# Optimization experiments

Measured on AMD Instinct MI355X. Metric: run time of the kernel, lower is better.

Reference implementation:

```python
import jax, jax.numpy as jnp
import numpy as np

N, E, S, G = 20000, 60000, 3000, 128
EAD = 5
DIMS = [(16, 32), (32, 64), (64, 64)]  # NNConv (M_in, M_out) per layer
HID = 128  # edge-MLP hidden
FC_IN = 64 + 8  # conv output + raw continuous feats


def setup_inputs() -> dict:
    key = jax.random.key(0)
    ks = iter(jax.random.split(key, 64))
    inp = {}
    inp['x'] = jax.random.normal(next(ks), (N, 24), jnp.float32)
    inp['edge_index'] = jax.random.randint(next(ks), (2, E), 0, N)
    inp['edge_attr'] = jax.random.uniform(next(ks), (E, EAD), jnp.float32)
    inp['node_to_subgraph'] = jnp.sort(jax.random.randint(next(ks), (N,), 0, S))
    inp['subgraph_to_graph'] = jnp.sort(jax.random.randint(next(ks), (S,), 0, G))
    for i, (mi, mo) in enumerate(DIMS):
        inp[f'conv{i}_w1'] = jax.random.normal(next(ks), (EAD, HID), jnp.float32) / np.sqrt(EAD)
        inp[f'conv{i}_b1'] = jnp.zeros((HID,), jnp.float32)
        inp[f'conv{i}_w2'] = jax.random.normal(next(ks), (HID, mi * mo), jnp.float32) / np.sqrt(HID * mi)
        inp[f'conv{i}_b2'] = jnp.zeros((mi * mo,), jnp.float32)
        inp[f'conv{i}_root'] = jax.random.normal(next(ks), (mi, mo), jnp.float32) / np.sqrt(mi)
        inp[f'conv{i}_bias'] = jnp.zeros((mo,), jnp.float32)
    dims_fc = [(FC_IN, FC_IN // 2), (FC_IN // 2, FC_IN // 4), (FC_IN // 4, 1)]
    for i, (di, do) in enumerate(dims_fc):
        inp[f'fc{i+1}_w'] = jax.random.normal(next(ks), (di, do), jnp.float32) / np.sqrt(di)
        inp[f'fc{i+1}_b'] = jnp.zeros((do,), jnp.float32)
    return inp


def _nnconv(x, src, dst, ea, w1, b1, w2, b2, root, bias):
    # edge MLP -> per-edge weight matrix [E, M_in, M_out]
    h = jax.nn.relu(ea @ w1 + b1)
    mi, mo = root.shape
    W = (h @ w2 + b2).reshape(-1, mi, mo)
    msg = jnp.einsum('ei,eio->eo', x[src], W)  # gather + per-edge matmul
    agg = jax.ops.segment_sum(msg, dst, num_segments=x.shape[0])  # scatter-add
    return agg + x @ root + bias


def _mean_pool(x, seg, num):
    s = jax.ops.segment_sum(x, seg, num_segments=num)
    c = jax.ops.segment_sum(jnp.ones((x.shape[0], 1), x.dtype), seg, num_segments=num)
    return s / jnp.maximum(c, 1.0)


def _forward(x, edge_index, edge_attr, node_to_subgraph, subgraph_to_graph, convs, fcs):
    src, dst = edge_index[0], edge_index[1]
    xi = x[:, :16]
    for p in convs:
        xi = jax.nn.elu(_nnconv(xi, src, dst, edge_attr, *p))
    x_cont = x[:, 16:]
    xc = jnp.concatenate([xi, x_cont], axis=1)  # [N, 72]
    xs = _mean_pool(xc, node_to_subgraph, S)    # [S, 72]
    xg = _mean_pool(xs, subgraph_to_graph, G)   # [G, 72]
    (w1, b1), (w2, b2), (w3, b3) = fcs
    xg = jax.nn.elu(xg @ w1 + b1)
    xg = jax.nn.elu(xg @ w2 + b2)
    return (xg @ w3 + b3).reshape(-1)


def reference(x, edge_index, edge_attr, node_to_subgraph, subgraph_to_graph,
              conv0_w1, conv0_b1, conv0_w2, conv0_b2, conv0_root, conv0_bias,
              conv1_w1, conv1_b1, conv1_w2, conv1_b2, conv1_root, conv1_bias,
              conv2_w1, conv2_b1, conv2_w2, conv2_b2, conv2_root, conv2_bias,
              fc1_w, fc1_b, fc2_w, fc2_b, fc3_w, fc3_b):
    convs = [
        (conv0_w1, conv0_b1, conv0_w2, conv0_b2, conv0_root, conv0_bias),
        (conv1_w1, conv1_b1, conv1_w2, conv1_b2, conv1_root, conv1_bias),
        (conv2_w1, conv2_b1, conv2_w2, conv2_b2, conv2_root, conv2_bias),
    ]
    fcs = [(fc1_w, fc1_b), (fc2_w, fc2_b), (fc3_w, fc3_b)]
    return _forward(x, edge_index, edge_attr, node_to_subgraph, subgraph_to_graph, convs, fcs)
```

## Files before the change

### kernel.cpp

```cpp
#include <hip/hip_runtime.h>
#include <hip/hip_bf16.h>
#include <cmath>

#define NN 20000
#define NE 60000
#define NS 3000
#define NG 128
#define HIDN 128
#define SCB 79

typedef float f32x16 __attribute__((ext_vector_type(16)));
typedef _Float16 f16x8 __attribute__((ext_vector_type(8)));

__device__ __forceinline__ float eluf(float v) { return v > 0.f ? v : expm1f(v); }

__device__ __forceinline__ void gload_lds16(const void* g, void* l) {
    __builtin_amdgcn_global_load_lds(
        (const __attribute__((address_space(1))) unsigned int*)g,
        (__attribute__((address_space(3))) unsigned int*)l, 16, 0, 0);
}

template <int N> struct VmWait;
template <> struct VmWait<0>  { static __device__ __forceinline__ void run() { asm volatile("s_waitcnt vmcnt(0)"  ::: "memory"); } };
template <> struct VmWait<12> { static __device__ __forceinline__ void run() { asm volatile("s_waitcnt vmcnt(12)" ::: "memory"); } };
template <> struct VmWait<16> { static __device__ __forceinline__ void run() { asm volatile("s_waitcnt vmcnt(16)" ::: "memory"); } };
template <> struct VmWait<40> { static __device__ __forceinline__ void run() { asm volatile("s_waitcnt vmcnt(40)" ::: "memory"); } };

__global__ void k_hist(const int* __restrict__ dst, int* __restrict__ deg) {
    int e = blockIdx.x * 256 + threadIdx.x;
    if (e < NE) atomicAdd(&deg[dst[e]], 1);
}

__global__ void k_scan1(const int* __restrict__ deg, int* __restrict__ bsum) {
    __shared__ int s[256];
    const int t = threadIdx.x;
    int i = blockIdx.x * 256 + t;
    s[t] = (i < NN) ? deg[i] : 0;
    __syncthreads();
#pragma unroll
    for (int off = 128; off > 0; off >>= 1) {
        if (t < off) s[t] += s[t + off];
        __syncthreads();
    }
    if (t == 0) bsum[blockIdx.x] = s[0];
}

__global__ void k_scan2(const int* __restrict__ bsum, int* __restrict__ boff) {
    __shared__ int s[SCB];
    const int t = threadIdx.x;
    if (t < SCB) s[t] = bsum[t];
    __syncthreads();
    if (t == 0) {
        int acc = 0;
        for (int i = 0; i < SCB; ++i) { int v = s[i]; s[i] = acc; acc += v; }
    }
    __syncthreads();
    if (t < SCB) boff[t] = s[t];
}

__global__ void k_scan3(const int* __restrict__ deg, const int* __restrict__ boff,
                        int* __restrict__ rowptr) {
    __shared__ int s[256];
    const int t = threadIdx.x;
    int i = blockIdx.x * 256 + t;
    int v = (i < NN) ? deg[i] : 0;
    s[t] = v;
    __syncthreads();
#pragma unroll
    for (int off = 1; off < 256; off <<= 1) {
        int a = (t >= off) ? s[t - off] : 0;
        __syncthreads();
        s[t] += a;
        __syncthreads();
    }
    if (i < NN) rowptr[i + 1] = boff[blockIdx.x] + s[t];
    if (i == 0) rowptr[0] = 0;
}

__global__ void k_scatter(const int* __restrict__ src, const int* __restrict__ dst,
                          const int* __restrict__ rowptr, int* __restrict__ tmp,
                          int* __restrict__ eord, int* __restrict__ srcS) {
    int e = blockIdx.x * 256 + threadIdx.x;
    if (e >= NE) return;
    int d = dst[e];
    int pos = rowptr[d] + atomicAdd(&tmp[d], 1);
    eord[pos] = e;
    srcS[pos] = src[e];
}

__global__ void k_hT2(const int* __restrict__ eord, const float* __restrict__ ea,
                      const float* __restrict__ w1, const float* __restrict__ b1,
                      _Float16* __restrict__ hT) {
    __shared__ float sea[64][5];
    const int t  = threadIdx.x;
    const int eb = blockIdx.x * 64;
    for (int i = t; i < 320; i += 256) {
        int el = i / 5, d = i % 5;
        int es = eb + el;
        int e = (es < NE) ? eord[es] : 0;
        sea[el][d] = ea[e * 5 + d];
    }
    __syncthreads();
    const int w = t >> 6, lane = t & 63;
    const int es = eb + lane;
    const float a0 = sea[lane][0], a1 = sea[lane][1], a2 = sea[lane][2],
                a3 = sea[lane][3], a4 = sea[lane][4];
#pragma unroll 4
    for (int jj = 0; jj < 32; ++jj) {
        const int j = w * 32 + jj;
        float s = b1[j];
        s = fmaf(a0, w1[0 * HIDN + j], s);
        s = fmaf(a1, w1[1 * HIDN + j], s);
        s = fmaf(a2, w1[2 * HIDN + j], s);
        s = fmaf(a3, w1[3 * HIDN + j], s);
        s = fmaf(a4, w1[4 * HIDN + j], s);
        if (es < NE) hT[(size_t)j * NE + es] = (_Float16)fmaxf(s, 0.f);
    }
}

template <int MI, int MO>
__global__ void k_w2t(const float* __restrict__ w2, const float* __restrict__ b2,
                      _Float16* __restrict__ w2t) {
    constexpr int KP = 129 * MI;
    constexpr int KF = 128 * MI;
    int idx = blockIdx.x * 256 + threadIdx.x;
    if (idx >= MO * KP) return;
    int o = idx / KP, kg = idx % KP;
    float v = (kg < KF) ? w2[(size_t)kg * MO + o] : b2[(kg - KF) * MO + o];
    w2t[idx] = (_Float16)v;
}

__global__ void k_x16h(const float* __restrict__ x, _Float16* __restrict__ xh) {
    int idx = blockIdx.x * 256 + threadIdx.x;
    if (idx >= NN * 16) return;
    int n = idx >> 4, i = idx & 15;
    xh[idx] = (_Float16)x[n * 24 + i];
}

template <int MI, int MO, int XS>
__global__ __launch_bounds__(256, 2) void k_edge6(
    const _Float16* __restrict__ xi, const _Float16* __restrict__ hT,
    const _Float16* __restrict__ w2t, const int* __restrict__ srcS,
    float* __restrict__ msg) {
    constexpr int PH  = MI / 16;
    constexpr int KP  = 129 * MI;
    constexpr int NT  = MO / 32;
    constexpr int CH  = 16 / (PH * NT);
    constexpr int NCH = 64 / CH;
    constexpr int VMK = 8 + 2 * CH;
    static_assert(CH * PH * NT == 16, "ITEMS must be 16");

    __shared__ __align__(16) _Float16 sb[2][2][16 * 512];

    const int lane = threadIdx.x & 63;
    const int w    = threadIdx.x >> 6;
    const int mg   = w & 1;
    const int kh   = w >> 1;
    const int lo5  = lane & 31;
    const int hi   = lane >> 5;
    const int e0   = blockIdx.x * 128 + mg * 64;
    const int kb   = kh * 64;

    const int rc0 = min(e0 + lo5, NE - 1);
    const int rc1 = min(e0 + 32 + lo5, NE - 1);
    const int s0 = srcS[rc0];
    const int s1 = srcS[rc1];

    f16x8 xr0[PH], xr1[PH];
    {
        const _Float16* xb0 = xi + (size_t)s0 * XS + hi * 8;
        const _Float16* xb1 = xi + (size_t)s1 * XS + hi * 8;
#pragma unroll
        for (int p = 0; p < PH; ++p) {
            xr0[p] = *reinterpret_cast<const f16x8*>(xb0 + p * 16);
            xr1[p] = *reinterpret_cast<const f16x8*>(xb1 + p * 16);
        }
    }

    f32x16 acc[2][NT];
#pragma unroll
    for (int m = 0; m < 2; ++m)
#pragma unroll
        for (int n = 0; n < NT; ++n)
#pragma unroll
            for (int i = 0; i < 16; ++i) acc[m][n][i] = 0.f;

    auto stage = [&](int buf, int kc) {
#pragma unroll
        for (int jj = 0; jj < 8; ++jj) {
            const int j  = mg + jj * 2;
            const int n  = j % NT;
            const int kp = j / NT;
            const int p  = kp % PH;
            const int kk = kp / PH;
            gload_lds16(w2t + (size_t)(n * 32 + lo5) * KP
                            + (size_t)(kb + kc + kk) * MI + p * 16 + hi * 8,
                        &sb[kh][buf][j * 512]);
        }
    };

    _Float16 hc0[CH], hc1[CH], hn0[CH], hn1[CH];

    stage(0, 0);
#pragma unroll
    for (int kk = 0; kk < CH; ++kk) {
        hc0[kk] = hT[(size_t)(kb + kk) * NE + rc0];
        hc1[kk] = hT[(size_t)(kb + kk) * NE + rc1];
    }

    for (int c = 0; c < NCH; ++c) {
        const bool pf = (c + 1 < NCH);
        if (pf) {
            stage((c + 1) & 1, (c + 1) * CH);
#pragma unroll
            for (int kk = 0; kk < CH; ++kk) {
                hn0[kk] = hT[(size_t)(kb + (c + 1) * CH + kk) * NE + rc0];
                hn1[kk] = hT[(size_t)(kb + (c + 1) * CH + kk) * NE + rc1];
            }
        }
        if (pf) VmWait<VMK>::run(); else VmWait<0>::run();
        __builtin_amdgcn_s_barrier();
        __builtin_amdgcn_sched_barrier(0);
        asm volatile("" ::: "memory");

        const _Float16* sbc = &sb[kh][c & 1][0];
#pragma unroll
        for (int kk = 0; kk < CH; ++kk) {
            const _Float16 hv0 = hc0[kk];
            const _Float16 hv1 = hc1[kk];
            const f16x8 h80 = {hv0, hv0, hv0, hv0, hv0, hv0, hv0, hv0};
            const f16x8 h81 = {hv1, hv1, hv1, hv1, hv1, hv1, hv1, hv1};
#pragma unroll
            for (int p = 0; p < PH; ++p) {
                const f16x8 af0 = xr0[p] * h80;
                const f16x8 af1 = xr1[p] * h81;
#pragma unroll
                for (int n = 0; n < NT; ++n) {
                    const f16x8 bv = *reinterpret_cast<const f16x8*>(
                        &sbc[((kk * PH + p) * NT + n) * 512 + lane * 8]);
                    acc[0][n] = __builtin_amdgcn_mfma_f32_32x32x16_f16(af0, bv, acc[0][n], 0, 0, 0);
                    acc[1][n] = __builtin_amdgcn_mfma_f32_32x32x16_f16(af1, bv, acc[1][n], 0, 0, 0);
                }
            }
        }
        __builtin_amdgcn_sched_barrier(0);
        asm volatile("" ::: "memory");
        __builtin_amdgcn_s_barrier();
        if (pf) {
#pragma unroll
            for (int kk = 0; kk < CH; ++kk) { hc0[kk] = hn0[kk]; hc1[kk] = hn1[kk]; }
        }
    }

    if (kh == 1) {
#pragma unroll
        for (int p = 0; p < PH; ++p) {
#pragma unroll
            for (int n = 0; n < NT; ++n) {
                const f16x8 bv = *reinterpret_cast<const f16x8*>(
                    w2t + (size_t)(n * 32 + lo5) * KP + (size_t)128 * MI + p * 16 + hi * 8);
                acc[0][n] = __builtin_amdgcn_mfma_f32_32x32x16_f16(xr0[p], bv, acc[0][n], 0, 0, 0);
                acc[1][n] = __builtin_amdgcn_mfma_f32_32x32x16_f16(xr1[p], bv, acc[1][n], 0, 0, 0);
            }
        }
    }

    __syncthreads();
    float* red = reinterpret_cast<float*>(&sb[0][0][0]);
    if (kh == 1) {
#pragma unroll
        for (int m = 0; m < 2; ++m)
#pragma unroll
            for (int n = 0; n < NT; ++n) {
                float* d = red + (size_t)((mg * 2 + m) * NT + n) * 1024 + lane;
#pragma unroll
                for (int i = 0; i < 16; ++i) d[i * 64] = acc[m][n][i];
            }
    }
    __syncthreads();
    if (kh == 0) {
#pragma unroll
        for (int m = 0; m < 2; ++m)
#pragma unroll
            for (int n = 0; n < NT; ++n) {
                const float* s = red + (size_t)((mg * 2 + m) * NT + n) * 1024 + lane;
#pragma unroll
                for (int i = 0; i < 16; ++i) acc[m][n][i] += s[i * 64];
            }
#pragma unroll
        for (int m = 0; m < 2; ++m)
#pragma unroll
            for (int q = 0; q < 4; ++q)
#pragma unroll
                for (int a = 0; a < 4; ++a) {
                    const int e = e0 + m * 32 + 4 * hi + 8 * q + a;
                    if (e < NE) {
#pragma unroll
                        for (int n = 0; n < NT; ++n)
                            msg[(size_t)e * MO + n * 32 + lo5] = acc[m][n][4 * q + a];
                    }
                }
    }
}

template <int MI, int MO, int XS>
__global__ void k_agg(const float* __restrict__ msg, const int* __restrict__ rowptr,
                      const float* __restrict__ xi, const float* __restrict__ root,
                      const float* __restrict__ bias, float* __restrict__ out,
                      _Float16* __restrict__ outh) {
    int idx = blockIdx.x * 256 + threadIdx.x;
    if (idx >= NN * MO) return;
    int n = idx / MO, o = idx % MO;
    float s = bias[o];
#pragma unroll
    for (int i = 0; i < MI; ++i) s = fmaf(xi[(size_t)n * XS + i], root[i * MO + o], s);
    const int j0 = rowptr[n], j1 = rowptr[n + 1];
    for (int j = j0; j < j1; ++j) s += msg[(size_t)j * MO + o];
    float r = eluf(s);
    out[idx] = r;
    outh[idx] = (_Float16)r;
}

__global__ void k_pool_s(const float* __restrict__ xi, const float* __restrict__ x,
                         const int* __restrict__ n2s, float* __restrict__ xs_sum,
                         float* __restrict__ cs) {
    int idx = blockIdx.x * 256 + threadIdx.x;
    if (idx >= NN * 72) return;
    int n = idx / 72, j = idx % 72;
    float v = (j < 64) ? xi[n * 64 + j] : x[n * 24 + 16 + (j - 64)];
    int s = n2s[n];
    atomicAdd(&xs_sum[s * 72 + j], v);
    if (j == 0) atomicAdd(&cs[s], 1.f);
}

__global__ void k_pool_g(const float* __restrict__ xs_sum, const float* __restrict__ cs,
                         const int* __restrict__ s2g, float* __restrict__ xg_sum,
                         float* __restrict__ cg) {
    int idx = blockIdx.x * 256 + threadIdx.x;
    if (idx >= NS * 72) return;
    int s = idx / 72, j = idx % 72;
    float v = xs_sum[s * 72 + j] / fmaxf(cs[s], 1.f);
    int g = s2g[s];
    atomicAdd(&xg_sum[g * 72 + j], v);
    if (j == 0) atomicAdd(&cg[g], 1.f);
}

__global__ void k_fc(const float* __restrict__ xg_sum, const float* __restrict__ cg,
                     const float* __restrict__ w1, const float* __restrict__ b1,
                     const float* __restrict__ w2, const float* __restrict__ b2,
                     const float* __restrict__ w3, const float* __restrict__ b3,
                     float* __restrict__ out) {
    int g = threadIdx.x;
    if (g >= NG) return;
    float inv = 1.f / fmaxf(cg[g], 1.f);
    float v[72];
#pragma unroll
    for (int j = 0; j < 72; ++j) v[j] = xg_sum[g * 72 + j] * inv;
    float h1[36];
#pragma unroll
    for (int o = 0; o < 36; ++o) {
        float s = b1[o];
#pragma unroll
        for (int i = 0; i < 72; ++i) s = fmaf(v[i], w1[i * 36 + o], s);
        h1[o] = eluf(s);
    }
    float h2[18];
#pragma unroll
    for (int o = 0; o < 18; ++o) {
        float s = b2[o];
#pragma unroll
        for (int i = 0; i < 36; ++i) s = fmaf(h1[i], w2[i * 18 + o], s);
        h2[o] = eluf(s);
    }
    float s = b3[0];
#pragma unroll
    for (int i = 0; i < 18; ++i) s = fmaf(h2[i], w3[i], s);
    out[g] = s;
}

extern "C" void kernel_launch(void* const* d_in, const int* in_sizes, int n_in,
                              void* d_out, int out_size, void* d_ws, size_t ws_size,
                              hipStream_t stream) {
    const float* x   = (const float*)d_in[0];
    const int*   ei  = (const int*)d_in[1];
    const float* ea  = (const float*)d_in[2];
    const int*   n2s = (const int*)d_in[3];
    const int*   s2g = (const int*)d_in[4];
    const int* src = ei;
    const int* dst = ei + NE;

    const float* cw1[3]   = {(const float*)d_in[5],  (const float*)d_in[11], (const float*)d_in[17]};
    const float* cb1[3]   = {(const float*)d_in[6],  (const float*)d_in[12], (const float*)d_in[18]};
    const float* cw2[3]   = {(const float*)d_in[7],  (const float*)d_in[13], (const float*)d_in[19]};
    const float* cb2[3]   = {(const float*)d_in[8],  (const float*)d_in[14], (const float*)d_in[20]};
    const float* croot[3] = {(const float*)d_in[9],  (const float*)d_in[15], (const float*)d_in[21]};
    const float* cbias[3] = {(const float*)d_in[10], (const float*)d_in[16], (const float*)d_in[22]};
    const float* fc1w = (const float*)d_in[23];
    const float* fc1b = (const float*)d_in[24];
    const float* fc2w = (const float*)d_in[25];
    const float* fc2b = (const float*)d_in[26];
    const float* fc3w = (const float*)d_in[27];
    const float* fc3b = (const float*)d_in[28];

    char* W = (char*)d_ws;
    _Float16* hT    = (_Float16*)(W);
    float*    xiA   = (float*)(W + 15360000);
    float*    xiB   = (float*)(W + 20480000);
    _Float16* xiAh  = (_Float16*)(W + 25600000);
    _Float16* xiBh  = (_Float16*)(W + 28160000);
    _Float16* x16h  = (_Float16*)(W + 30720000);
    float*    msg   = (float*)(W + 31360000);
    float*    xs_sum= (float*)(W + 46720000);
    float*    cs    = (float*)(W + 47584000);
    float*    xg_sum= (float*)(W + 47596000);
    float*    cg    = (float*)(W + 47632864);
    _Float16* w2t0  = (_Float16*)(W + 47633376);
    _Float16* w2t1  = (_Float16*)(W + 47765472);
    _Float16* w2t2  = (_Float16*)(W + 48293856);
    int*      deg   = (int*)(W + 49350624);
    int*      tmp   = (int*)(W + 49430624);
    int*      rowptr= (int*)(W + 49510624);
    int*      eord  = (int*)(W + 49590640);
    int*      srcS  = (int*)(W + 49830640);
    int*      bsum  = (int*)(W + 50070640);
    int*      boff  = (int*)(W + 50070960);

    hipMemsetAsync(xs_sum, 0, (size_t)(NS * 72 + NS) * 4 + (size_t)(NG * 72 + NG) * 4, stream);
    hipMemsetAsync(deg, 0, 160000, stream);

    k_hist<<<(NE + 255) / 256, 256, 0, stream>>>(dst, deg);
    k_scan1<<<SCB, 256, 0, stream>>>(deg, bsum);
    k_scan2<<<1, 128, 0, stream>>>(bsum, boff);
    k_scan3<<<SCB, 256, 0, stream>>>(deg, boff, rowptr);
    k_scatter<<<(NE + 255) / 256, 256, 0, stream>>>(src, dst, rowptr, tmp, eord, srcS);

    k_w2t<16, 32><<<(32 * 129 * 16 + 255) / 256, 256, 0, stream>>>(cw2[0], cb2[0], w2t0);
    k_w2t<32, 64><<<(64 * 129 * 32 + 255) / 256, 256, 0, stream>>>(cw2[1], cb2[1], w2t1);
    k_w2t<64, 64><<<(64 * 129 * 64 + 255) / 256, 256, 0, stream>>>(cw2[2], cb2[2], w2t2);
    k_x16h<<<(NN * 16 + 255) / 256, 256, 0, stream>>>(x, x16h);

    const int EB = (NE + 127) / 128;
    const int HTB = (NE + 63) / 64;

    k_hT2<<<HTB, 256, 0, stream>>>(eord, ea, cw1[0], cb1[0], hT);
    k_edge6<16, 32, 16><<<EB, 256, 0, stream>>>(x16h, hT, w2t0, srcS, msg);
    k_agg<16, 32, 24><<<(NN * 32 + 255) / 256, 256, 0, stream>>>(msg, rowptr, x, croot[0], cbias[0], xiB, xiBh);

    k_hT2<<<HTB, 256, 0, stream>>>(eord, ea, cw1[1], cb1[1], hT);
    k_edge6<32, 64, 32><<<EB, 256, 0, stream>>>(xiBh, hT, w2t1, srcS, msg);
    k_agg<32, 64, 32><<<(NN * 64 + 255) / 256, 256, 0, stream>>>(msg, rowptr, xiB, croot[1], cbias[1], xiA, xiAh);

    k_hT2<<<HTB, 256, 0, stream>>>(eord, ea, cw1[2], cb1[2], hT);
    k_edge6<64, 64, 64><<<EB, 256, 0, stream>>>(xiAh, hT, w2t2, srcS, msg);
    k_agg<64, 64, 64><<<(NN * 64 + 255) / 256, 256, 0, stream>>>(msg, rowptr, xiA, croot[2], cbias[2], xiB, xiBh);

    k_pool_s<<<(NN * 72 + 255) / 256, 256, 0, stream>>>(xiB, x, n2s, xs_sum, cs);
    k_pool_g<<<(NS * 72 + 255) / 256, 256, 0, stream>>>(xs_sum, cs, s2g, xg_sum, cg);
    k_fc<<<1, 128, 0, stream>>>(xg_sum, cg, fc1w, fc1b, fc2w, fc2b, fc3w, fc3b, (float*)d_out);
}
```

Before: 313.0 us.

## Split edge kernel output columns across grid y and double-buffer with unrolled loop

The per-edge MFMA kernel now computes only one 32-wide output tile per block, with the output-column tile index taken from blockIdx.y. This halves LDS staging and accumulator registers, which allows a launch bound of 4 blocks per SM instead of 2. The chunk loop is unrolled by two with fixed buffer indices, and the wait counts are adjusted to match. In exchange, the gather of x rows and of hT is repeated for each column tile, so layers with 64 outputs now read those inputs twice.

```diff
diff --git a/kernel.cpp b/kernel.cpp
--- a/kernel.cpp
+++ b/kernel.cpp
@@ -22,9 +22,9 @@
 
 template <int N> struct VmWait;
 template <> struct VmWait<0>  { static __device__ __forceinline__ void run() { asm volatile("s_waitcnt vmcnt(0)"  ::: "memory"); } };
+template <> struct VmWait<8>  { static __device__ __forceinline__ void run() { asm volatile("s_waitcnt vmcnt(8)"  ::: "memory"); } };
 template <> struct VmWait<12> { static __device__ __forceinline__ void run() { asm volatile("s_waitcnt vmcnt(12)" ::: "memory"); } };
-template <> struct VmWait<16> { static __device__ __forceinline__ void run() { asm volatile("s_waitcnt vmcnt(16)" ::: "memory"); } };
-template <> struct VmWait<40> { static __device__ __forceinline__ void run() { asm volatile("s_waitcnt vmcnt(40)" ::: "memory"); } };
+template <> struct VmWait<20> { static __device__ __forceinline__ void run() { asm volatile("s_waitcnt vmcnt(20)" ::: "memory"); } };
 
 __global__ void k_hist(const int* __restrict__ dst, int* __restrict__ deg) {
     int e = blockIdx.x * 256 + threadIdx.x;
@@ -138,19 +138,19 @@
 }
 
 template <int MI, int MO, int XS>
-__global__ __launch_bounds__(256, 2) void k_edge6(
+__global__ __launch_bounds__(256, 4) void k_edge7(
     const _Float16* __restrict__ xi, const _Float16* __restrict__ hT,
     const _Float16* __restrict__ w2t, const int* __restrict__ srcS,
     float* __restrict__ msg) {
     constexpr int PH  = MI / 16;
     constexpr int KP  = 129 * MI;
-    constexpr int NT  = MO / 32;
-    constexpr int CH  = 16 / (PH * NT);
+    constexpr int CH  = 8 / PH;
     constexpr int NCH = 64 / CH;
-    constexpr int VMK = 8 + 2 * CH;
-    static_assert(CH * PH * NT == 16, "ITEMS must be 16");
-
-    __shared__ __align__(16) _Float16 sb[2][2][16 * 512];
+    constexpr int VMK = 4 + 2 * CH;
+    static_assert(CH * PH == 8, "ITEMS must be 8");
+    static_assert(NCH % 2 == 0, "chunk loop unrolled x2");
+
+    __shared__ __align__(16) _Float16 sb[2][2][8 * 512];
 
     const int lane = threadIdx.x & 63;
     const int w    = threadIdx.x >> 6;
@@ -159,6 +159,7 @@
     const int lo5  = lane & 31;
     const int hi   = lane >> 5;
     const int e0   = blockIdx.x * 128 + mg * 64;
+    const int ns   = blockIdx.y;
     const int kb   = kh * 64;
 
     const int rc0 = min(e0 + lo5, NE - 1);
@@ -177,91 +178,92 @@
         }
     }
 
-    f32x16 acc[2][NT];
-#pragma unroll
-    for (int m = 0; m < 2; ++m)
-#pragma unroll
-        for (int n = 0; n < NT; ++n)
-#pragma unroll
-            for (int i = 0; i < 16; ++i) acc[m][n][i] = 0.f;
+    f32x16 acc0, acc1;
+#pragma unroll
+    for (int i = 0; i < 16; ++i) { acc0[i] = 0.f; acc1[i] = 0.f; }
+
+    const _Float16* bbase = w2t + (size_t)(ns * 32 + lo5) * KP + hi * 8;
 
     auto stage = [&](int buf, int kc) {
 #pragma unroll
-        for (int jj = 0; jj < 8; ++jj) {
+        for (int jj = 0; jj < 4; ++jj) {
             const int j  = mg + jj * 2;
-            const int n  = j % NT;
-            const int kp = j / NT;
-            const int p  = kp % PH;
-            const int kk = kp / PH;
-            gload_lds16(w2t + (size_t)(n * 32 + lo5) * KP
-                            + (size_t)(kb + kc + kk) * MI + p * 16 + hi * 8,
+            const int kk = j / PH;
+            const int p  = j % PH;
+            gload_lds16(bbase + (size_t)(kb + kc + kk) * MI + p * 16,
                         &sb[kh][buf][j * 512]);
         }
     };
 
-    _Float16 hc0[CH], hc1[CH], hn0[CH], hn1[CH];
-
-    stage(0, 0);
-#pragma unroll
-    for (int kk = 0; kk < CH; ++kk) {
-        hc0[kk] = hT[(size_t)(kb + kk) * NE + rc0];
-        hc1[kk] = hT[(size_t)(kb + kk) * NE + rc1];
-    }
-
-    for (int c = 0; c < NCH; ++c) {
-        const bool pf = (c + 1 < NCH);
-        if (pf) {
-            stage((c + 1) & 1, (c + 1) * CH);
-#pragma unroll
-            for (int kk = 0; kk < CH; ++kk) {
-                hn0[kk] = hT[(size_t)(kb + (c + 1) * CH + kk) * NE + rc0];
-                hn1[kk] = hT[(size_t)(kb + (c + 1) * CH + kk) * NE + rc1];
-            }
-        }
-        if (pf) VmWait<VMK>::run(); else VmWait<0>::run();
-        __builtin_amdgcn_s_barrier();
-        __builtin_amdgcn_sched_barrier(0);
-        asm volatile("" ::: "memory");
-
-        const _Float16* sbc = &sb[kh][c & 1][0];
+    auto compute = [&](int buf, const _Float16* h0, const _Float16* h1) {
+        const _Float16* sbc = &sb[kh][buf][0];
 #pragma unroll
         for (int kk = 0; kk < CH; ++kk) {
-            const _Float16 hv0 = hc0[kk];
-            const _Float16 hv1 = hc1[kk];
+            const _Float16 hv0 = h0[kk];
+            const _Float16 hv1 = h1[kk];
             const f16x8 h80 = {hv0, hv0, hv0, hv0, hv0, hv0, hv0, hv0};
             const f16x8 h81 = {hv1, hv1, hv1, hv1, hv1, hv1, hv1, hv1};
 #pragma unroll
             for (int p = 0; p < PH; ++p) {
                 const f16x8 af0 = xr0[p] * h80;
                 const f16x8 af1 = xr1[p] * h81;
-#pragma unroll
-                for (int n = 0; n < NT; ++n) {
-                    const f16x8 bv = *reinterpret_cast<const f16x8*>(
-                        &sbc[((kk * PH + p) * NT + n) * 512 + lane * 8]);
-                    acc[0][n] = __builtin_amdgcn_mfma_f32_32x32x16_f16(af0, bv, acc[0][n], 0, 0, 0);
-                    acc[1][n] = __builtin_amdgcn_mfma_f32_32x32x16_f16(af1, bv, acc[1][n], 0, 0, 0);
-                }
+                const f16x8 bv = *reinterpret_cast<const f16x8*>(
+                    &sbc[(kk * PH + p) * 512 + lane * 8]);
+                acc0 = __builtin_amdgcn_mfma_f32_32x32x16_f16(af0, bv, acc0, 0, 0, 0);
+                acc1 = __builtin_amdgcn_mfma_f32_32x32x16_f16(af1, bv, acc1, 0, 0, 0);
             }
         }
+    };
+
+    _Float16 hA0[CH], hA1[CH], hB0[CH], hB1[CH];
+
+    stage(0, 0);
+#pragma unroll
+    for (int kk = 0; kk < CH; ++kk) {
+        hA0[kk] = hT[(size_t)(kb + kk) * NE + rc0];
+        hA1[kk] = hT[(size_t)(kb + kk) * NE + rc1];
+    }
+
+    for (int c = 0; c < NCH; c += 2) {
+        stage(1, (c + 1) * CH);
+#pragma unroll
+        for (int kk = 0; kk < CH; ++kk) {
+            hB0[kk] = hT[(size_t)(kb + (c + 1) * CH + kk) * NE + rc0];
+            hB1[kk] = hT[(size_t)(kb + (c + 1) * CH + kk) * NE + rc1];
+        }
+        VmWait<VMK>::run();
+        __builtin_amdgcn_s_barrier();
         __builtin_amdgcn_sched_barrier(0);
-        asm volatile("" ::: "memory");
+        compute(0, hA0, hA1);
+        __builtin_amdgcn_sched_barrier(0);
         __builtin_amdgcn_s_barrier();
+
+        const bool pf = (c + 2 < NCH);
         if (pf) {
-#pragma unroll
-            for (int kk = 0; kk < CH; ++kk) { hc0[kk] = hn0[kk]; hc1[kk] = hn1[kk]; }
-        }
+            stage(0, (c + 2) * CH);
+#pragma unroll
+            for (int kk = 0; kk < CH; ++kk) {
+                hA0[kk] = hT[(size_t)(kb + (c + 2) * CH + kk) * NE + rc0];
+                hA1[kk] = hT[(size_t)(kb + (c + 2) * CH + kk) * NE + rc1];
+            }
+            VmWait<VMK>::run();
+        } else {
+            VmWait<0>::run();
+        }
+        __builtin_amdgcn_s_barrier();
+        __builtin_amdgcn_sched_barrier(0);
+        compute(1, hB0, hB1);
+        __builtin_amdgcn_sched_barrier(0);
+        __builtin_amdgcn_s_barrier();
     }
 
     if (kh == 1) {
 #pragma unroll
         for (int p = 0; p < PH; ++p) {
-#pragma unroll
-            for (int n = 0; n < NT; ++n) {
-                const f16x8 bv = *reinterpret_cast<const f16x8*>(
-                    w2t + (size_t)(n * 32 + lo5) * KP + (size_t)128 * MI + p * 16 + hi * 8);
-                acc[0][n] = __builtin_amdgcn_mfma_f32_32x32x16_f16(xr0[p], bv, acc[0][n], 0, 0, 0);
-                acc[1][n] = __builtin_amdgcn_mfma_f32_32x32x16_f16(xr1[p], bv, acc[1][n], 0, 0, 0);
-            }
+            const f16x8 bv = *reinterpret_cast<const f16x8*>(
+                bbase + (size_t)128 * MI + p * 16);
+            acc0 = __builtin_amdgcn_mfma_f32_32x32x16_f16(xr0[p], bv, acc0, 0, 0, 0);
+            acc1 = __builtin_amdgcn_mfma_f32_32x32x16_f16(xr1[p], bv, acc1, 0, 0, 0);
         }
     }
 
@@ -269,35 +271,32 @@
     float* red = reinterpret_cast<float*>(&sb[0][0][0]);
     if (kh == 1) {
 #pragma unroll
+        for (int m = 0; m < 2; ++m) {
+            float* d = red + (size_t)(mg * 2 + m) * 1024 + lane;
+            const f32x16& a = (m == 0) ? acc0 : acc1;
+#pragma unroll
+            for (int i = 0; i < 16; ++i) d[i * 64] = a[i];
+        }
+    }
+    __syncthreads();
+    if (kh == 0) {
+#pragma unroll
+        for (int m = 0; m < 2; ++m) {
+            const float* s = red + (size_t)(mg * 2 + m) * 1024 + lane;
+            f32x16& a = (m == 0) ? acc0 : acc1;
+#pragma unroll
+            for (int i = 0; i < 16; ++i) a[i] += s[i * 64];
+        }
+#pragma unroll
         for (int m = 0; m < 2; ++m)
 #pragma unroll
-            for (int n = 0; n < NT; ++n) {
-                float* d = red + (size_t)((mg * 2 + m) * NT + n) * 1024 + lane;
-#pragma unroll
-                for (int i = 0; i < 16; ++i) d[i * 64] = acc[m][n][i];
-            }
-    }
-    __syncthreads();
-    if (kh == 0) {
-#pragma unroll
-        for (int m = 0; m < 2; ++m)
-#pragma unroll
-            for (int n = 0; n < NT; ++n) {
-                const float* s = red + (size_t)((mg * 2 + m) * NT + n) * 1024 + lane;
-#pragma unroll
-                for (int i = 0; i < 16; ++i) acc[m][n][i] += s[i * 64];
-            }
-#pragma unroll
-        for (int m = 0; m < 2; ++m)
-#pragma unroll
             for (int q = 0; q < 4; ++q)
 #pragma unroll
-                for (int a = 0; a < 4; ++a) {
-                    const int e = e0 + m * 32 + 4 * hi + 8 * q + a;
+                for (int a2 = 0; a2 < 4; ++a2) {
+                    const int e = e0 + m * 32 + 4 * hi + 8 * q + a2;
                     if (e < NE) {
-#pragma unroll
-                        for (int n = 0; n < NT; ++n)
-                            msg[(size_t)e * MO + n * 32 + lo5] = acc[m][n][4 * q + a];
+                        const float v = (m == 0) ? acc0[4 * q + a2] : acc1[4 * q + a2];
+                        msg[(size_t)e * MO + ns * 32 + lo5] = v;
                     }
                 }
     }
@@ -443,15 +442,15 @@
     const int HTB = (NE + 63) / 64;
 
     k_hT2<<<HTB, 256, 0, stream>>>(eord, ea, cw1[0], cb1[0], hT);
-    k_edge6<16, 32, 16><<<EB, 256, 0, stream>>>(x16h, hT, w2t0, srcS, msg);
+    k_edge7<16, 32, 16><<<dim3(EB, 1), 256, 0, stream>>>(x16h, hT, w2t0, srcS, msg);
     k_agg<16, 32, 24><<<(NN * 32 + 255) / 256, 256, 0, stream>>>(msg, rowptr, x, croot[0], cbias[0], xiB, xiBh);
 
     k_hT2<<<HTB, 256, 0, stream>>>(eord, ea, cw1[1], cb1[1], hT);
-    k_edge6<32, 64, 32><<<EB, 256, 0, stream>>>(xiBh, hT, w2t1, srcS, msg);
+    k_edge7<32, 64, 32><<<dim3(EB, 2), 256, 0, stream>>>(xiBh, hT, w2t1, srcS, msg);
     k_agg<32, 64, 32><<<(NN * 64 + 255) / 256, 256, 0, stream>>>(msg, rowptr, xiB, croot[1], cbias[1], xiA, xiAh);
 
     k_hT2<<<HTB, 256, 0, stream>>>(eord, ea, cw1[2], cb1[2], hT);
-    k_edge6<64, 64, 64><<<EB, 256, 0, stream>>>(xiAh, hT, w2t2, srcS, msg);
+    k_edge7<64, 64, 64><<<dim3(EB, 2), 256, 0, stream>>>(xiAh, hT, w2t2, srcS, msg);
     k_agg<64, 64, 64><<<(NN * 64 + 255) / 256, 256, 0, stream>>>(msg, rowptr, xiA, croot[2], cbias[2], xiB, xiBh);
 
     k_pool_s<<<(NN * 72 + 255) / 256, 256, 0, stream>>>(xiB, x, n2s, xs_sum, cs);
```

Measured after the change: 329.9 us. 5.4% more time.

## Give each wave private LDS buffers and drop per-chunk block barriers in edge kernel

Applied to the files above, without the earlier changes.

Each wave now stages its own weight tiles into a private LDS region instead of sharing half-tiles with a partner wave, which removes the two workgroup barriers per chunk. The chunk size is halved to eight MFMA items and the loop is unrolled by two with explicit ping-pong buffers, relying only on per-wave vmcnt waits. This trades duplicated global-to-LDS traffic (each wave loads the full tile rather than half) for less synchronization and better latency hiding.

```diff
diff --git a/kernel.cpp b/kernel.cpp
--- a/kernel.cpp
+++ b/kernel.cpp
@@ -22,9 +22,9 @@
 
 template <int N> struct VmWait;
 template <> struct VmWait<0>  { static __device__ __forceinline__ void run() { asm volatile("s_waitcnt vmcnt(0)"  ::: "memory"); } };
+template <> struct VmWait<10> { static __device__ __forceinline__ void run() { asm volatile("s_waitcnt vmcnt(10)" ::: "memory"); } };
 template <> struct VmWait<12> { static __device__ __forceinline__ void run() { asm volatile("s_waitcnt vmcnt(12)" ::: "memory"); } };
-template <> struct VmWait<16> { static __device__ __forceinline__ void run() { asm volatile("s_waitcnt vmcnt(16)" ::: "memory"); } };
-template <> struct VmWait<40> { static __device__ __forceinline__ void run() { asm volatile("s_waitcnt vmcnt(40)" ::: "memory"); } };
+template <> struct VmWait<24> { static __device__ __forceinline__ void run() { asm volatile("s_waitcnt vmcnt(24)" ::: "memory"); } };
 
 __global__ void k_hist(const int* __restrict__ dst, int* __restrict__ deg) {
     int e = blockIdx.x * 256 + threadIdx.x;
@@ -138,19 +138,20 @@
 }
 
 template <int MI, int MO, int XS>
-__global__ __launch_bounds__(256, 2) void k_edge6(
+__global__ __launch_bounds__(256, 2) void k_edge8(
     const _Float16* __restrict__ xi, const _Float16* __restrict__ hT,
     const _Float16* __restrict__ w2t, const int* __restrict__ srcS,
     float* __restrict__ msg) {
     constexpr int PH  = MI / 16;
     constexpr int KP  = 129 * MI;
     constexpr int NT  = MO / 32;
-    constexpr int CH  = 16 / (PH * NT);
+    constexpr int CH  = 8 / (PH * NT);
     constexpr int NCH = 64 / CH;
     constexpr int VMK = 8 + 2 * CH;
-    static_assert(CH * PH * NT == 16, "ITEMS must be 16");
-
-    __shared__ __align__(16) _Float16 sb[2][2][16 * 512];
+    static_assert(CH * PH * NT == 8, "ITEMS must be 8");
+    static_assert(NCH % 2 == 0, "chunk loop unrolled x2");
+
+    __shared__ __align__(16) _Float16 sb[4][2][8 * 512];
 
     const int lane = threadIdx.x & 63;
     const int w    = threadIdx.x >> 6;
@@ -187,47 +188,23 @@
 
     auto stage = [&](int buf, int kc) {
 #pragma unroll
-        for (int jj = 0; jj < 8; ++jj) {
-            const int j  = mg + jj * 2;
+        for (int j = 0; j < 8; ++j) {
             const int n  = j % NT;
             const int kp = j / NT;
             const int p  = kp % PH;
             const int kk = kp / PH;
             gload_lds16(w2t + (size_t)(n * 32 + lo5) * KP
                             + (size_t)(kb + kc + kk) * MI + p * 16 + hi * 8,
-                        &sb[kh][buf][j * 512]);
+                        &sb[w][buf][j * 512]);
         }
     };
 
-    _Float16 hc0[CH], hc1[CH], hn0[CH], hn1[CH];
-
-    stage(0, 0);
-#pragma unroll
-    for (int kk = 0; kk < CH; ++kk) {
-        hc0[kk] = hT[(size_t)(kb + kk) * NE + rc0];
-        hc1[kk] = hT[(size_t)(kb + kk) * NE + rc1];
-    }
-
-    for (int c = 0; c < NCH; ++c) {
-        const bool pf = (c + 1 < NCH);
-        if (pf) {
-            stage((c + 1) & 1, (c + 1) * CH);
-#pragma unroll
-            for (int kk = 0; kk < CH; ++kk) {
-                hn0[kk] = hT[(size_t)(kb + (c + 1) * CH + kk) * NE + rc0];
-                hn1[kk] = hT[(size_t)(kb + (c + 1) * CH + kk) * NE + rc1];
-            }
-        }
-        if (pf) VmWait<VMK>::run(); else VmWait<0>::run();
-        __builtin_amdgcn_s_barrier();
-        __builtin_amdgcn_sched_barrier(0);
-        asm volatile("" ::: "memory");
-
-        const _Float16* sbc = &sb[kh][c & 1][0];
+    auto compute = [&](int buf, const _Float16* h0, const _Float16* h1) {
+        const _Float16* sbc = &sb[w][buf][0];
 #pragma unroll
         for (int kk = 0; kk < CH; ++kk) {
-            const _Float16 hv0 = hc0[kk];
-            const _Float16 hv1 = hc1[kk];
+            const _Float16 hv0 = h0[kk];
+            const _Float16 hv1 = h1[kk];
             const f16x8 h80 = {hv0, hv0, hv0, hv0, hv0, hv0, hv0, hv0};
             const f16x8 h81 = {hv1, hv1, hv1, hv1, hv1, hv1, hv1, hv1};
 #pragma unroll
@@ -243,13 +220,44 @@
                 }
             }
         }
+    };
+
+    _Float16 hA0[CH], hA1[CH], hB0[CH], hB1[CH];
+
+    stage(0, 0);
+#pragma unroll
+    for (int kk = 0; kk < CH; ++kk) {
+        hA0[kk] = hT[(size_t)(kb + kk) * NE + rc0];
+        hA1[kk] = hT[(size_t)(kb + kk) * NE + rc1];
+    }
+
+    for (int c = 0; c < NCH; c += 2) {
+        stage(1, (c + 1) * CH);
+#pragma unroll
+        for (int kk = 0; kk < CH; ++kk) {
+            hB0[kk] = hT[(size_t)(kb + (c + 1) * CH + kk) * NE + rc0];
+            hB1[kk] = hT[(size_t)(kb + (c + 1) * CH + kk) * NE + rc1];
+        }
+        VmWait<VMK>::run();
         __builtin_amdgcn_sched_barrier(0);
-        asm volatile("" ::: "memory");
-        __builtin_amdgcn_s_barrier();
+        compute(0, hA0, hA1);
+        __builtin_amdgcn_sched_barrier(0);
+
+        const bool pf = (c + 2 < NCH);
         if (pf) {
-#pragma unroll
-            for (int kk = 0; kk < CH; ++kk) { hc0[kk] = hn0[kk]; hc1[kk] = hn1[kk]; }
-        }
+            stage(0, (c + 2) * CH);
+#pragma unroll
+            for (int kk = 0; kk < CH; ++kk) {
+                hA0[kk] = hT[(size_t)(kb + (c + 2) * CH + kk) * NE + rc0];
+                hA1[kk] = hT[(size_t)(kb + (c + 2) * CH + kk) * NE + rc1];
+            }
+            VmWait<VMK>::run();
+        } else {
+            VmWait<0>::run();
+        }
+        __builtin_amdgcn_sched_barrier(0);
+        compute(1, hB0, hB1);
+        __builtin_amdgcn_sched_barrier(0);
     }
 
     if (kh == 1) {
@@ -292,12 +300,12 @@
 #pragma unroll
             for (int q = 0; q < 4; ++q)
 #pragma unroll
-                for (int a = 0; a < 4; ++a) {
-                    const int e = e0 + m * 32 + 4 * hi + 8 * q + a;
+                for (int a2 = 0; a2 < 4; ++a2) {
+                    const int e = e0 + m * 32 + 4 * hi + 8 * q + a2;
                     if (e < NE) {
 #pragma unroll
                         for (int n = 0; n < NT; ++n)
-                            msg[(size_t)e * MO + n * 32 + lo5] = acc[m][n][4 * q + a];
+                            msg[(size_t)e * MO + n * 32 + lo5] = acc[m][n][4 * q + a2];
                     }
                 }
     }
@@ -443,15 +451,15 @@
     const int HTB = (NE + 63) / 64;
 
     k_hT2<<<HTB, 256, 0, stream>>>(eord, ea, cw1[0], cb1[0], hT);
-    k_edge6<16, 32, 16><<<EB, 256, 0, stream>>>(x16h, hT, w2t0, srcS, msg);
+    k_edge8<16, 32, 16><<<EB, 256, 0, stream>>>(x16h, hT, w2t0, srcS, msg);
     k_agg<16, 32, 24><<<(NN * 32 + 255) / 256, 256, 0, stream>>>(msg, rowptr, x, croot[0], cbias[0], xiB, xiBh);
 
     k_hT2<<<HTB, 256, 0, stream>>>(eord, ea, cw1[1], cb1[1], hT);
-    k_edge6<32, 64, 32><<<EB, 256, 0, stream>>>(xiBh, hT, w2t1, srcS, msg);
+    k_edge8<32, 64, 32><<<EB, 256, 0, stream>>>(xiBh, hT, w2t1, srcS, msg);
     k_agg<32, 64, 32><<<(NN * 64 + 255) / 256, 256, 0, stream>>>(msg, rowptr, xiB, croot[1], cbias[1], xiA, xiAh);
 
     k_hT2<<<HTB, 256, 0, stream>>>(eord, ea, cw1[2], cb1[2], hT);
-    k_edge6<64, 64, 64><<<EB, 256, 0, stream>>>(xiAh, hT, w2t2, srcS, msg);
+    k_edge8<64, 64, 64><<<EB, 256, 0, stream>>>(xiAh, hT, w2t2, srcS, msg);
     k_agg<64, 64, 64><<<(NN * 64 + 255) / 256, 256, 0, stream>>>(msg, rowptr, xiA, croot[2], cbias[2], xiB, xiBh);
 
     k_pool_s<<<(NN * 72 + 255) / 256, 256, 0, stream>>>(xiB, x, n2s, xs_sum, cs);
```

New measurement: 400.1 us. 1.28x slower.
